# Performance work log

Measured on AMD Instinct MI355X. Metric: run time of the kernel, lower is better.

Reference implementation:

```python
import jax, jax.numpy as jnp
import numpy as np


def _segment_mean(x, idx, num_segments):
    # mean-aggregate rows of x into num_segments buckets (PyG SAGEConv default aggr)
    s = jax.ops.segment_sum(x, idx, num_segments=num_segments)
    c = jax.ops.segment_sum(jnp.ones((idx.shape[0],), x.dtype), idx, num_segments=num_segments)
    return s / jnp.maximum(c, 1.0)[:, None]


def setup_inputs() -> dict:
    key = jax.random.key(0)
    ks = jax.random.split(key, 12)
    N_LIG, N_PROT, D, H, E = 100000, 50000, 64, 128, 2000000
    sc = 0.05
    return {
        "x_lig": jax.random.normal(ks[0], (N_LIG, D), jnp.float32),
        "x_prot": jax.random.normal(ks[1], (N_PROT, D), jnp.float32),
        "W_l_lp": jax.random.normal(ks[2], (D, H), jnp.float32) * sc,
        "b_lp": jnp.zeros((H,), jnp.float32),
        "W_r_lp": jax.random.normal(ks[3], (D, H), jnp.float32) * sc,
        "W_l_pl": jax.random.normal(ks[4], (D, H), jnp.float32) * sc,
        "b_pl": jnp.zeros((H,), jnp.float32),
        "W_r_pl": jax.random.normal(ks[5], (D, H), jnp.float32) * sc,
        "W_lin": jax.random.normal(ks[6], (H, 1), jnp.float32) * sc,
        "b_lin": jnp.zeros((1,), jnp.float32),
        "src_lp": jax.random.randint(ks[7], (E,), 0, N_LIG, jnp.int32),
        "dst_lp": jax.random.randint(ks[8], (E,), 0, N_PROT, jnp.int32),
        "src_pl": jax.random.randint(ks[9], (E,), 0, N_PROT, jnp.int32),
        "dst_pl": jax.random.randint(ks[10], (E,), 0, N_LIG, jnp.int32),
    }


def reference(x_lig, x_prot, W_l_lp, b_lp, W_r_lp, W_l_pl, b_pl, W_r_pl,
              W_lin, b_lin, src_lp, dst_lp, src_pl, dst_pl):
    n_lig = x_lig.shape[0]
    n_prot = x_prot.shape[0]
    # SAGEConv ('ligand','interacts','protein'): gather ligand feats along edges, mean into proteins
    agg_prot = _segment_mean(x_lig[src_lp], dst_lp, n_prot)          # [N_prot, D]
    h_prot = jax.nn.relu(agg_prot @ W_l_lp + b_lp + x_prot @ W_r_lp)  # [N_prot, H] (dead downstream, as in original)
    # SAGEConv ('protein','interacts','ligand')
    agg_lig = _segment_mean(x_prot[src_pl], dst_pl, n_lig)           # [N_lig, D]
    h_lig = jax.nn.relu(agg_lig @ W_l_pl + b_pl + x_lig @ W_r_pl)    # [N_lig, H]
    ligand_out = h_lig.mean(axis=0)                                  # [H]
    del h_prot  # original computes it but never uses it (only 'ligand' feeds the head)
    return ligand_out @ W_lin + b_lin                                # [1]
```

## Files before the change

### kernel.cpp

```cpp
#include <hip/hip_runtime.h>

#define D 64
#define H 128
#define BN 128
#define CAP 3456
#define NBB 512
#define CE 3908

typedef short bf16x8 __attribute__((ext_vector_type(8)));
typedef float f32x4  __attribute__((ext_vector_type(4)));
typedef float f32x2  __attribute__((ext_vector_type(2)));

__device__ __forceinline__ ushort f2bf(float f) {
    unsigned u = __float_as_uint(f);
    unsigned r = (u + 0x7FFFu + ((u >> 16) & 1u)) >> 16;
    return (ushort)r;
}

__device__ __forceinline__ bf16x8 pack8v(f32x4 a, f32x4 b) {
    ushort o[8];
    o[0]=f2bf(a[0]); o[1]=f2bf(a[1]); o[2]=f2bf(a[2]); o[3]=f2bf(a[3]);
    o[4]=f2bf(b[0]); o[5]=f2bf(b[1]); o[6]=f2bf(b[2]); o[7]=f2bf(b[3]);
    bf16x8 r;
    __builtin_memcpy(&r, o, 16);
    return r;
}

__device__ __forceinline__ void acc16(f32x2* a, uint4 v) {
    a[0] += __builtin_amdgcn_cvt_pk_f32_fp8((int)v.x, false);
    a[1] += __builtin_amdgcn_cvt_pk_f32_fp8((int)v.x, true);
    a[2] += __builtin_amdgcn_cvt_pk_f32_fp8((int)v.y, false);
    a[3] += __builtin_amdgcn_cvt_pk_f32_fp8((int)v.y, true);
    a[4] += __builtin_amdgcn_cvt_pk_f32_fp8((int)v.z, false);
    a[5] += __builtin_amdgcn_cvt_pk_f32_fp8((int)v.z, true);
    a[6] += __builtin_amdgcn_cvt_pk_f32_fp8((int)v.w, false);
    a[7] += __builtin_amdgcn_cvt_pk_f32_fp8((int)v.w, true);
}

__device__ __forceinline__ unsigned pk4_fp8(float x0, float x1, float x2, float x3) {
    int w = __builtin_amdgcn_cvt_pk_fp8_f32(x0, x1, 0, false);
    w = __builtin_amdgcn_cvt_pk_fp8_f32(x2, x3, w, true);
    return (unsigned)w;
}

__device__ __forceinline__ int wave_incl_scan(int v, int lane) {
    #pragma unroll
    for (int o = 1; o < 64; o <<= 1) {
        int x = __shfl_up(v, o);
        if (lane >= o) v += x;
    }
    return v;
}

__global__ __launch_bounds__(256)
void stage1_kernel(const float* __restrict__ xp, unsigned char* __restrict__ xp8, int totalp,
                   const float* __restrict__ Wl, const float* __restrict__ Wr,
                   ushort* __restrict__ wprep,
                   const int* __restrict__ dst, int* __restrict__ cnt,
                   int E, int K, int ce, int PB) {
    __shared__ int scnt[800];
    int bid = blockIdx.x;
    int t = threadIdx.x;
    if (bid < PB) {
        int i = (bid * 256 + t) * 16;
        if (i < totalp) {
            const f32x4* p = (const f32x4*)(xp + i);
            f32x4 a = __builtin_nontemporal_load(p);
            f32x4 b = __builtin_nontemporal_load(p + 1);
            f32x4 c = __builtin_nontemporal_load(p + 2);
            f32x4 d = __builtin_nontemporal_load(p + 3);
            uint4 o;
            o.x = pk4_fp8(a[0], a[1], a[2], a[3]);
            o.y = pk4_fp8(b[0], b[1], b[2], b[3]);
            o.z = pk4_fp8(c[0], c[1], c[2], c[3]);
            o.w = pk4_fp8(d[0], d[1], d[2], d[3]);
            *(uint4*)(xp8 + i) = o;
        }
    } else if (bid < PB + 8) {
        int e = (bid - PB) * 256 + t;
        if (e < 2048) {
            int lane = e & 63;
            int ks = (e >> 6) & 3;
            int ht = e >> 8;
            int h = ht * 16 + (lane & 15);
            int kgp = lane >> 4;
            ushort o[8];
            #pragma unroll
            for (int j = 0; j < 8; ++j) {
                int k = (ks < 2) ? (kgp * 16 + ks * 8 + j)
                                 : (ks * 32 + kgp * 8 + j);
                float v = (k < D) ? Wl[k * H + h] : Wr[(k - D) * H + h];
                o[j] = f2bf(v);
            }
            *(bf16x8*)(wprep + (size_t)e * 8) = *(bf16x8*)o;
        }
    } else {
        int blk = bid - PB - 8;
        for (int b = t; b < 800; b += 256) scnt[b] = 0;
        __syncthreads();
        int e0 = blk * ce;
        int e1 = min(E, e0 + ce);
        for (int i = e0 + t * 4; i < e1; i += 1024) {
            int4 d4 = *(const int4*)(dst + i);
            atomicAdd(&scnt[d4.x >> 7], 1);
            atomicAdd(&scnt[d4.y >> 7], 1);
            atomicAdd(&scnt[d4.z >> 7], 1);
            atomicAdd(&scnt[d4.w >> 7], 1);
        }
        __syncthreads();
        int* row = cnt + (size_t)blk * K;
        for (int b = t; b < K; b += 256) row[b] = scnt[b];
    }
}

__global__ __launch_bounds__(NBB)
void part_scan_kernel(const int* __restrict__ cnt, int* __restrict__ off,
                      int* __restrict__ tot, int K) {
    __shared__ int wsum[NBB / 64];
    int b = blockIdx.x;
    int t = threadIdx.x;
    int lane = t & 63, wv = t >> 6;
    int v = cnt[(size_t)t * K + b];
    int incl = wave_incl_scan(v, lane);
    if (lane == 63) wsum[wv] = incl;
    __syncthreads();
    int add = 0;
    #pragma unroll
    for (int w = 0; w < NBB / 64; ++w)
        if (w < wv) add += wsum[w];
    off[(size_t)t * K + b] = incl + add - v;
    if (t == NBB - 1) tot[b] = incl + add;
}

__global__ __launch_bounds__(512)
void part_scatter_kernel(const int* __restrict__ src, const int* __restrict__ dst,
                         const int* __restrict__ off, int* __restrict__ gb,
                         int E, int K, int ce) {
    __shared__ int shist[800];
    __shared__ int sbase[800];
    __shared__ int gdelta[800];
    __shared__ int lcur[800];
    __shared__ int sscan[512];
    __shared__ int ebuf[CE];
    __shared__ unsigned short bkt[CE];

    int blk = blockIdx.x, t = threadIdx.x;
    int e0 = blk * ce;
    int e1 = min(E, e0 + ce);
    int myn = e1 - e0;

    for (int b = t; b < 800; b += 512) shist[b] = 0;
    __syncthreads();
    for (int i = e0 + t * 4; i < e1; i += 2048) {
        int4 d4 = *(const int4*)(dst + i);
        atomicAdd(&shist[d4.x >> 7], 1);
        atomicAdd(&shist[d4.y >> 7], 1);
        atomicAdd(&shist[d4.z >> 7], 1);
        atomicAdd(&shist[d4.w >> 7], 1);
    }
    __syncthreads();
    int c0 = 0, c1 = 0;
    if (t < 400) { c0 = shist[2 * t]; c1 = shist[2 * t + 1]; }
    int cs = c0 + c1;
    sscan[t] = (t < 400) ? cs : 0;
    __syncthreads();
    for (int o = 1; o < 512; o <<= 1) {
        int x = (t >= o) ? sscan[t - o] : 0;
        __syncthreads();
        sscan[t] += x;
        __syncthreads();
    }
    if (t < 400) {
        int ex = sscan[t] - cs;
        sbase[2 * t] = ex;
        sbase[2 * t + 1] = ex + c0;
    }
    __syncthreads();
    const int* orow = off + (size_t)blk * K;
    for (int b = t; b < K; b += 512) {
        int sb = sbase[b];
        gdelta[b] = orow[b] - sb;
        lcur[b] = sb;
    }
    __syncthreads();
    for (int i = e0 + t * 4; i < e1; i += 2048) {
        int4 d4 = *(const int4*)(dst + i);
        int4 s4 = *(const int4*)(src + i);
        int b, p;
        b = d4.x >> 7; p = atomicAdd(&lcur[b], 1);
        ebuf[p] = (s4.x & 0xFFFF) | ((d4.x & 127) << 16); bkt[p] = (unsigned short)b;
        b = d4.y >> 7; p = atomicAdd(&lcur[b], 1);
        ebuf[p] = (s4.y & 0xFFFF) | ((d4.y & 127) << 16); bkt[p] = (unsigned short)b;
        b = d4.z >> 7; p = atomicAdd(&lcur[b], 1);
        ebuf[p] = (s4.z & 0xFFFF) | ((d4.z & 127) << 16); bkt[p] = (unsigned short)b;
        b = d4.w >> 7; p = atomicAdd(&lcur[b], 1);
        ebuf[p] = (s4.w & 0xFFFF) | ((d4.w & 127) << 16); bkt[p] = (unsigned short)b;
    }
    __syncthreads();
    for (int p = t; p < myn; p += 512) {
        int b = bkt[p];
        int loc = gdelta[b] + p;
        if (loc < CAP) gb[(size_t)b * CAP + loc] = ebuf[p];
    }
}

__global__ __launch_bounds__(512, 6)
void fused_kernel(const unsigned char* __restrict__ xp8, const float* __restrict__ x_lig,
                  const int* __restrict__ gtot, const int* __restrict__ gb,
                  const ushort* __restrict__ wprep, const float* __restrict__ bvec,
                  float* __restrict__ pgrid, int N) {
    __shared__ int sdeg[BN];
    __shared__ int sstart[BN];
    __shared__ int scur[BN];
    __shared__ int swtot[2];
    __shared__ int scsr[CAP];
    __shared__ float sred[8][H];

    int b = blockIdx.x, t = threadIdx.x;
    int wv = t >> 6, lane = t & 63;
    int cnt = min(gtot[b], CAP);
    const int* mygb = gb + (size_t)b * CAP;

    if (t < BN) sdeg[t] = 0;
    __syncthreads();
    for (int i = t; i < cnt; i += 512)
        atomicAdd(&sdeg[__builtin_nontemporal_load(&mygb[i]) >> 16], 1);
    __syncthreads();
    int inclv = 0, degv = 0;
    if (t < BN) {
        degv = sdeg[t];
        inclv = wave_incl_scan(degv, lane);
        if (lane == 63) swtot[wv] = inclv;
    }
    __syncthreads();
    if (t < BN) {
        int ex = inclv + ((t >= 64) ? swtot[0] : 0) - degv;
        sstart[t] = ex;
        scur[t] = ex;
    }
    __syncthreads();
    for (int i = t; i < cnt; i += 512) {
        int e = __builtin_nontemporal_load(&mygb[i]);
        int p = atomicAdd(&scur[e >> 16], 1);
        scsr[p] = e & 0xFFFF;
    }
    __syncthreads();

    int r = lane & 15, kg = lane >> 4;

    int ln = wv * 16 + r;
    int s0 = sstart[ln], dg = sdeg[ln];
    f32x2 a[8];
    #pragma unroll
    for (int k = 0; k < 8; ++k) { a[k][0] = 0.f; a[k][1] = 0.f; }
    int j = 0;
    for (; j + 3 < dg; j += 4) {
        int i0 = scsr[s0 + j];
        int i1 = scsr[s0 + j + 1];
        int i2 = scsr[s0 + j + 2];
        int i3 = scsr[s0 + j + 3];
        uint4 v0 = *((const uint4*)(xp8 + (size_t)i0 * D) + kg);
        uint4 v1 = *((const uint4*)(xp8 + (size_t)i1 * D) + kg);
        uint4 v2 = *((const uint4*)(xp8 + (size_t)i2 * D) + kg);
        uint4 v3 = *((const uint4*)(xp8 + (size_t)i3 * D) + kg);
        acc16(a, v0); acc16(a, v1); acc16(a, v2); acc16(a, v3);
    }
    for (; j < dg; ++j) {
        int i0 = scsr[s0 + j];
        uint4 v0 = *((const uint4*)(xp8 + (size_t)i0 * D) + kg);
        acc16(a, v0);
    }

    float inv = 1.0f / fmaxf((float)dg, 1.0f);
    ushort o0[8], o1[8];
    #pragma unroll
    for (int k = 0; k < 4; ++k) {
        o0[2*k]   = f2bf(a[k][0] * inv);
        o0[2*k+1] = f2bf(a[k][1] * inv);
        o1[2*k]   = f2bf(a[4+k][0] * inv);
        o1[2*k+1] = f2bf(a[4+k][1] * inv);
    }
    bf16x8 A0, A1;
    __builtin_memcpy(&A0, o0, 16);
    __builtin_memcpy(&A1, o1, 16);

    int grow = b * BN + wv * 16 + r;
    bf16x8 A2, A3;
    if (grow < N) {
        const f32x4* xr = (const f32x4*)(x_lig + (size_t)grow * D);
        f32x4 va = __builtin_nontemporal_load(xr + kg * 2);
        f32x4 vb = __builtin_nontemporal_load(xr + kg * 2 + 1);
        A2 = pack8v(va, vb);
        f32x4 vc = __builtin_nontemporal_load(xr + 8 + kg * 2);
        f32x4 vd = __builtin_nontemporal_load(xr + 8 + kg * 2 + 1);
        A3 = pack8v(vc, vd);
    } else {
        A2 = bf16x8{0,0,0,0,0,0,0,0};
        A3 = A2;
    }

    float hsum[8];
    bool full = (b * BN + wv * 16 + 16 <= N);
    const bf16x8* wp = (const bf16x8*)wprep;
    #pragma unroll 2
    for (int ht = 0; ht < 8; ++ht) {
        f32x4 acc = {0.f, 0.f, 0.f, 0.f};
        acc = __builtin_amdgcn_mfma_f32_16x16x32_bf16(A0, wp[(ht*4+0)*64 + lane], acc, 0, 0, 0);
        acc = __builtin_amdgcn_mfma_f32_16x16x32_bf16(A1, wp[(ht*4+1)*64 + lane], acc, 0, 0, 0);
        acc = __builtin_amdgcn_mfma_f32_16x16x32_bf16(A2, wp[(ht*4+2)*64 + lane], acc, 0, 0, 0);
        acc = __builtin_amdgcn_mfma_f32_16x16x32_bf16(A3, wp[(ht*4+3)*64 + lane], acc, 0, 0, 0);
        float bb = bvec[ht * 16 + r];
        float s = 0.f;
        if (full) {
            #pragma unroll
            for (int i = 0; i < 4; ++i) s += fmaxf(acc[i] + bb, 0.f);
        } else {
            #pragma unroll
            for (int i = 0; i < 4; ++i) {
                int row = b * BN + wv * 16 + kg * 4 + i;
                if (row < N) s += fmaxf(acc[i] + bb, 0.f);
            }
        }
        hsum[ht] = s;
    }

    #pragma unroll
    for (int ht = 0; ht < 8; ++ht) {
        float v = hsum[ht];
        v += __shfl_xor(v, 16);
        v += __shfl_xor(v, 32);
        if (lane < 16) sred[wv][ht * 16 + lane] = v;
    }
    __syncthreads();
    if (t < H) {
        float s = 0.f;
        #pragma unroll
        for (int w = 0; w < 8; ++w) s += sred[w][t];
        pgrid[(size_t)b * H + t] = s;
    }
}

__global__ __launch_bounds__(128)
void reduce1_kernel(const float* __restrict__ pgrid, int nb, float* __restrict__ pgrid2) {
    int t = threadIdx.x;
    float s = 0.f;
    for (int r = blockIdx.x; r < nb; r += 64) s += pgrid[(size_t)r * H + t];
    pgrid2[(size_t)blockIdx.x * H + t] = s;
}

__global__ __launch_bounds__(128)
void head_kernel(const float* __restrict__ pgrid2,
                 const float* __restrict__ W_lin, const float* __restrict__ b_lin,
                 float* __restrict__ out, float invN) {
    __shared__ float sh[H];
    int t = threadIdx.x;
    float s = 0.f;
    #pragma unroll 8
    for (int r = 0; r < 64; ++r) s += pgrid2[(size_t)r * H + t];
    sh[t] = s * invN * W_lin[t];
    __syncthreads();
    if (t == 0) {
        float tot = b_lin[0];
        for (int i = 0; i < H; ++i) tot += sh[i];
        out[0] = tot;
    }
}

extern "C" void kernel_launch(void* const* d_in, const int* in_sizes, int n_in,
                              void* d_out, int out_size, void* d_ws, size_t ws_size,
                              hipStream_t stream) {
    const float* x_lig  = (const float*)d_in[0];
    const float* x_prot = (const float*)d_in[1];
    const float* W_l_pl = (const float*)d_in[5];
    const float* b_pl   = (const float*)d_in[6];
    const float* W_r_pl = (const float*)d_in[7];
    const float* W_lin  = (const float*)d_in[8];
    const float* b_lin  = (const float*)d_in[9];
    const int*   src_pl = (const int*)d_in[12];
    const int*   dst_pl = (const int*)d_in[13];

    int N  = in_sizes[0] / D;
    int NP = in_sizes[1] / D;
    int E  = in_sizes[12];
    int K  = (N + BN - 1) / BN;

    char* base = (char*)d_ws;
    unsigned char* xp8 = (unsigned char*)base; base += (size_t)NP * D;
    float* pgrid  = (float*)base;   base += (size_t)K * H * sizeof(float);
    float* pgrid2 = (float*)base;   base += (size_t)64 * H * sizeof(float);
    ushort* wprep = (ushort*)base;  base += (size_t)2048 * 8 * sizeof(ushort);
    int* cnt      = (int*)base;     base += (size_t)NBB * K * sizeof(int);
    int* off      = (int*)base;     base += (size_t)NBB * K * sizeof(int);
    int* tot      = (int*)base;     base += (size_t)K * sizeof(int);
    base = (char*)(((size_t)base + 255) & ~(size_t)255);
    int* gb       = (int*)base;     base += (size_t)K * CAP * sizeof(int);

    int ce = ((E + NBB - 1) / NBB + 3) & ~3;
    int PB = (NP * D / 16 + 255) / 256;

    stage1_kernel<<<PB + 8 + NBB, 256, 0, stream>>>(x_prot, xp8, NP * D,
                                                    W_l_pl, W_r_pl, wprep,
                                                    dst_pl, cnt, E, K, ce, PB);
    part_scan_kernel<<<K, NBB, 0, stream>>>(cnt, off, tot, K);
    part_scatter_kernel<<<NBB, 512, 0, stream>>>(src_pl, dst_pl, off, gb, E, K, ce);
    fused_kernel<<<K, 512, 0, stream>>>(xp8, x_lig, tot, gb, wprep, b_pl, pgrid, N);
    reduce1_kernel<<<64, 128, 0, stream>>>(pgrid, K, pgrid2);
    head_kernel<<<1, 128, 0, stream>>>(pgrid2, W_lin, b_lin, (float*)d_out,
                                       1.0f / (float)N);
}
```

Measured before the change: 85.06 us.

## Split each destination bucket across two 256-thread blocks and halve partition blocks

The fused aggregation kernel now launches two 256-thread blocks per 128-row bucket. Each block filters the bucket's edge list to its own 64-row half, builds a smaller shared CSR, and writes its own partial row of the per-block sum grid. NBB also drops from 512 to 256, which gives fewer, larger partition chunks in the scatter stages. The split is meant to raise occupancy and reduce shared memory per block, at the cost of each block reading the full bucket edge list twice. The new CAP2 limit on the shared CSR could drop edges if one half-bucket exceeds 1600 entries.

```diff
diff --git a/kernel.cpp b/kernel.cpp
--- a/kernel.cpp
+++ b/kernel.cpp
@@ -4,8 +4,9 @@
 #define H 128
 #define BN 128
 #define CAP 3456
-#define NBB 512
-#define CE 3908
+#define CAP2 1600
+#define NBB 256
+#define CE 7816
 
 typedef short bf16x8 __attribute__((ext_vector_type(8)));
 typedef float f32x4  __attribute__((ext_vector_type(4)));
@@ -204,48 +205,49 @@
     }
 }
 
-__global__ __launch_bounds__(512, 6)
+__global__ __launch_bounds__(256, 8)
 void fused_kernel(const unsigned char* __restrict__ xp8, const float* __restrict__ x_lig,
                   const int* __restrict__ gtot, const int* __restrict__ gb,
                   const ushort* __restrict__ wprep, const float* __restrict__ bvec,
                   float* __restrict__ pgrid, int N) {
-    __shared__ int sdeg[BN];
-    __shared__ int sstart[BN];
-    __shared__ int scur[BN];
-    __shared__ int swtot[2];
-    __shared__ int scsr[CAP];
-    __shared__ float sred[8][H];
-
-    int b = blockIdx.x, t = threadIdx.x;
-    int wv = t >> 6, lane = t & 63;
-    int cnt = min(gtot[b], CAP);
-    const int* mygb = gb + (size_t)b * CAP;
-
-    if (t < BN) sdeg[t] = 0;
-    __syncthreads();
-    for (int i = t; i < cnt; i += 512)
-        atomicAdd(&sdeg[__builtin_nontemporal_load(&mygb[i]) >> 16], 1);
-    __syncthreads();
-    int inclv = 0, degv = 0;
-    if (t < BN) {
-        degv = sdeg[t];
-        inclv = wave_incl_scan(degv, lane);
-        if (lane == 63) swtot[wv] = inclv;
-    }
-    __syncthreads();
-    if (t < BN) {
-        int ex = inclv + ((t >= 64) ? swtot[0] : 0) - degv;
-        sstart[t] = ex;
-        scur[t] = ex;
-    }
-    __syncthreads();
-    for (int i = t; i < cnt; i += 512) {
+    __shared__ int sdeg[64];
+    __shared__ int sstart[64];
+    __shared__ int scur[64];
+    __shared__ int scsr[CAP2];
+    __shared__ float sred[4][H];
+
+    int blk = blockIdx.x, t = threadIdx.x;
+    int bucket = blk >> 1, half = blk & 1;
+    int cnt = min(gtot[bucket], CAP);
+    const int* mygb = gb + (size_t)bucket * CAP;
+
+    if (t < 64) sdeg[t] = 0;
+    __syncthreads();
+    for (int i = t; i < cnt; i += 256) {
         int e = __builtin_nontemporal_load(&mygb[i]);
-        int p = atomicAdd(&scur[e >> 16], 1);
-        scsr[p] = e & 0xFFFF;
-    }
-    __syncthreads();
-
+        int lb = e >> 16;
+        if ((lb >> 6) == half) atomicAdd(&sdeg[lb & 63], 1);
+    }
+    __syncthreads();
+    int lane = t & 63;
+    if (t < 64) {
+        int degv = sdeg[t];
+        int incl = wave_incl_scan(degv, lane);
+        sstart[t] = incl - degv;
+        scur[t] = incl - degv;
+    }
+    __syncthreads();
+    for (int i = t; i < cnt; i += 256) {
+        int e = __builtin_nontemporal_load(&mygb[i]);
+        int lb = e >> 16;
+        if ((lb >> 6) == half) {
+            int p = atomicAdd(&scur[lb & 63], 1);
+            if (p < CAP2) scsr[p] = e & 0xFFFF;
+        }
+    }
+    __syncthreads();
+
+    int wv = t >> 6;
     int r = lane & 15, kg = lane >> 4;
 
     int ln = wv * 16 + r;
@@ -284,7 +286,7 @@
     __builtin_memcpy(&A0, o0, 16);
     __builtin_memcpy(&A1, o1, 16);
 
-    int grow = b * BN + wv * 16 + r;
+    int grow = blk * 64 + wv * 16 + r;
     bf16x8 A2, A3;
     if (grow < N) {
         const f32x4* xr = (const f32x4*)(x_lig + (size_t)grow * D);
@@ -300,7 +302,7 @@
     }
 
     float hsum[8];
-    bool full = (b * BN + wv * 16 + 16 <= N);
+    bool full = (blk * 64 + wv * 16 + 16 <= N);
     const bf16x8* wp = (const bf16x8*)wprep;
     #pragma unroll 2
     for (int ht = 0; ht < 8; ++ht) {
@@ -317,7 +319,7 @@
         } else {
             #pragma unroll
             for (int i = 0; i < 4; ++i) {
-                int row = b * BN + wv * 16 + kg * 4 + i;
+                int row = blk * 64 + wv * 16 + kg * 4 + i;
                 if (row < N) s += fmaxf(acc[i] + bb, 0.f);
             }
         }
@@ -333,10 +335,8 @@
     }
     __syncthreads();
     if (t < H) {
-        float s = 0.f;
-        #pragma unroll
-        for (int w = 0; w < 8; ++w) s += sred[w][t];
-        pgrid[(size_t)b * H + t] = s;
+        float s = sred[0][t] + sred[1][t] + sred[2][t] + sred[3][t];
+        pgrid[(size_t)blk * H + t] = s;
     }
 }
 
@@ -383,10 +383,11 @@
     int NP = in_sizes[1] / D;
     int E  = in_sizes[12];
     int K  = (N + BN - 1) / BN;
+    int K2 = K * 2;
 
     char* base = (char*)d_ws;
     unsigned char* xp8 = (unsigned char*)base; base += (size_t)NP * D;
-    float* pgrid  = (float*)base;   base += (size_t)K * H * sizeof(float);
+    float* pgrid  = (float*)base;   base += (size_t)K2 * H * sizeof(float);
     float* pgrid2 = (float*)base;   base += (size_t)64 * H * sizeof(float);
     ushort* wprep = (ushort*)base;  base += (size_t)2048 * 8 * sizeof(ushort);
     int* cnt      = (int*)base;     base += (size_t)NBB * K * sizeof(int);
@@ -403,8 +404,8 @@
                                                     dst_pl, cnt, E, K, ce, PB);
     part_scan_kernel<<<K, NBB, 0, stream>>>(cnt, off, tot, K);
     part_scatter_kernel<<<NBB, 512, 0, stream>>>(src_pl, dst_pl, off, gb, E, K, ce);
-    fused_kernel<<<K, 512, 0, stream>>>(xp8, x_lig, tot, gb, wprep, b_pl, pgrid, N);
-    reduce1_kernel<<<64, 128, 0, stream>>>(pgrid, K, pgrid2);
+    fused_kernel<<<K2, 256, 0, stream>>>(xp8, x_lig, tot, gb, wprep, b_pl, pgrid, N);
+    reduce1_kernel<<<64, 128, 0, stream>>>(pgrid, K2, pgrid2);
     head_kernel<<<1, 128, 0, stream>>>(pgrid2, W_lin, b_lin, (float*)d_out,
                                        1.0f / (float)N);
 }
```

New measurement: 110.7 us. 30.1% more time.

## Prefetch edge data into registers and hoist x_lig loads ahead of gather

Applied to the files above, without the earlier changes.

Halves the number of partition blocks (each now handles twice as many edges) and loads all dst indices into registers once, so the histogram and scatter passes reuse them instead of reading global memory twice. In the fused kernel, bucket entries are prefetched into registers before the histogram, so the CSR build reads them once. The x_lig row loads are issued before the neighbor gather loop so their latency overlaps it, and that loop's unroll drops from 4 to 2 to save registers. The trade-offs are higher register pressure, fewer partition blocks, and the fixed register counts (4 int4 per thread, 7 entries) must stay consistent with CE and CAP.

```diff
diff --git a/kernel.cpp b/kernel.cpp
--- a/kernel.cpp
+++ b/kernel.cpp
@@ -4,8 +4,8 @@
 #define H 128
 #define BN 128
 #define CAP 3456
-#define NBB 512
-#define CE 3908
+#define NBB 256
+#define CE 7816
 
 typedef short bf16x8 __attribute__((ext_vector_type(8)));
 typedef float f32x4  __attribute__((ext_vector_type(4)));
@@ -149,14 +149,23 @@
     int e1 = min(E, e0 + ce);
     int myn = e1 - e0;
 
+    int4 dreg[4];
+    #pragma unroll
+    for (int k = 0; k < 4; ++k) {
+        int i = e0 + (t + k * 512) * 4;
+        dreg[k] = (i < e1) ? *(const int4*)(dst + i) : make_int4(-1, -1, -1, -1);
+    }
+
     for (int b = t; b < 800; b += 512) shist[b] = 0;
     __syncthreads();
-    for (int i = e0 + t * 4; i < e1; i += 2048) {
-        int4 d4 = *(const int4*)(dst + i);
-        atomicAdd(&shist[d4.x >> 7], 1);
-        atomicAdd(&shist[d4.y >> 7], 1);
-        atomicAdd(&shist[d4.z >> 7], 1);
-        atomicAdd(&shist[d4.w >> 7], 1);
+    #pragma unroll
+    for (int k = 0; k < 4; ++k) {
+        if (dreg[k].x >= 0) {
+            atomicAdd(&shist[dreg[k].x >> 7], 1);
+            atomicAdd(&shist[dreg[k].y >> 7], 1);
+            atomicAdd(&shist[dreg[k].z >> 7], 1);
+            atomicAdd(&shist[dreg[k].w >> 7], 1);
+        }
     }
     __syncthreads();
     int c0 = 0, c1 = 0;
@@ -183,18 +192,21 @@
         lcur[b] = sb;
     }
     __syncthreads();
-    for (int i = e0 + t * 4; i < e1; i += 2048) {
-        int4 d4 = *(const int4*)(dst + i);
-        int4 s4 = *(const int4*)(src + i);
-        int b, p;
-        b = d4.x >> 7; p = atomicAdd(&lcur[b], 1);
-        ebuf[p] = (s4.x & 0xFFFF) | ((d4.x & 127) << 16); bkt[p] = (unsigned short)b;
-        b = d4.y >> 7; p = atomicAdd(&lcur[b], 1);
-        ebuf[p] = (s4.y & 0xFFFF) | ((d4.y & 127) << 16); bkt[p] = (unsigned short)b;
-        b = d4.z >> 7; p = atomicAdd(&lcur[b], 1);
-        ebuf[p] = (s4.z & 0xFFFF) | ((d4.z & 127) << 16); bkt[p] = (unsigned short)b;
-        b = d4.w >> 7; p = atomicAdd(&lcur[b], 1);
-        ebuf[p] = (s4.w & 0xFFFF) | ((d4.w & 127) << 16); bkt[p] = (unsigned short)b;
+    #pragma unroll
+    for (int k = 0; k < 4; ++k) {
+        int i = e0 + (t + k * 512) * 4;
+        if (dreg[k].x >= 0) {
+            int4 s4 = *(const int4*)(src + i);
+            int b, p;
+            b = dreg[k].x >> 7; p = atomicAdd(&lcur[b], 1);
+            ebuf[p] = (s4.x & 0xFFFF) | ((dreg[k].x & 127) << 16); bkt[p] = (unsigned short)b;
+            b = dreg[k].y >> 7; p = atomicAdd(&lcur[b], 1);
+            ebuf[p] = (s4.y & 0xFFFF) | ((dreg[k].y & 127) << 16); bkt[p] = (unsigned short)b;
+            b = dreg[k].z >> 7; p = atomicAdd(&lcur[b], 1);
+            ebuf[p] = (s4.z & 0xFFFF) | ((dreg[k].z & 127) << 16); bkt[p] = (unsigned short)b;
+            b = dreg[k].w >> 7; p = atomicAdd(&lcur[b], 1);
+            ebuf[p] = (s4.w & 0xFFFF) | ((dreg[k].w & 127) << 16); bkt[p] = (unsigned short)b;
+        }
     }
     __syncthreads();
     for (int p = t; p < myn; p += 512) {
@@ -221,12 +233,20 @@
     int cnt = min(gtot[b], CAP);
     const int* mygb = gb + (size_t)b * CAP;
 
+    int ev[7];
+    #pragma unroll
+    for (int k = 0; k < 7; ++k) {
+        int i = t + k * 512;
+        ev[k] = (i < cnt) ? __builtin_nontemporal_load(&mygb[i]) : -1;
+    }
+
     if (t < BN) sdeg[t] = 0;
     __syncthreads();
-    for (int i = t; i < cnt; i += 512)
-        atomicAdd(&sdeg[__builtin_nontemporal_load(&mygb[i]) >> 16], 1);
-    __syncthreads();
-    int inclv = 0, degv = 0;
+    #pragma unroll
+    for (int k = 0; k < 7; ++k)
+        if (ev[k] >= 0) atomicAdd(&sdeg[ev[k] >> 16], 1);
+    __syncthreads();
+    int degv = 0, inclv = 0;
     if (t < BN) {
         degv = sdeg[t];
         inclv = wave_incl_scan(degv, lane);
@@ -239,14 +259,25 @@
         scur[t] = ex;
     }
     __syncthreads();
-    for (int i = t; i < cnt; i += 512) {
-        int e = __builtin_nontemporal_load(&mygb[i]);
-        int p = atomicAdd(&scur[e >> 16], 1);
-        scsr[p] = e & 0xFFFF;
-    }
+    #pragma unroll
+    for (int k = 0; k < 7; ++k)
+        if (ev[k] >= 0) {
+            int p = atomicAdd(&scur[ev[k] >> 16], 1);
+            scsr[p] = ev[k] & 0xFFFF;
+        }
     __syncthreads();
 
     int r = lane & 15, kg = lane >> 4;
+
+    int grow = b * BN + wv * 16 + r;
+    f32x4 va = {0.f,0.f,0.f,0.f}, vb = va, vc = va, vd = va;
+    if (grow < N) {
+        const f32x4* xr = (const f32x4*)(x_lig + (size_t)grow * D);
+        va = __builtin_nontemporal_load(xr + kg * 2);
+        vb = __builtin_nontemporal_load(xr + kg * 2 + 1);
+        vc = __builtin_nontemporal_load(xr + 8 + kg * 2);
+        vd = __builtin_nontemporal_load(xr + 8 + kg * 2 + 1);
+    }
 
     int ln = wv * 16 + r;
     int s0 = sstart[ln], dg = sdeg[ln];
@@ -254,18 +285,15 @@
     #pragma unroll
     for (int k = 0; k < 8; ++k) { a[k][0] = 0.f; a[k][1] = 0.f; }
     int j = 0;
-    for (; j + 3 < dg; j += 4) {
+    for (; j + 1 < dg; j += 2) {
         int i0 = scsr[s0 + j];
         int i1 = scsr[s0 + j + 1];
-        int i2 = scsr[s0 + j + 2];
-        int i3 = scsr[s0 + j + 3];
         uint4 v0 = *((const uint4*)(xp8 + (size_t)i0 * D) + kg);
         uint4 v1 = *((const uint4*)(xp8 + (size_t)i1 * D) + kg);
-        uint4 v2 = *((const uint4*)(xp8 + (size_t)i2 * D) + kg);
-        uint4 v3 = *((const uint4*)(xp8 + (size_t)i3 * D) + kg);
-        acc16(a, v0); acc16(a, v1); acc16(a, v2); acc16(a, v3);
-    }
-    for (; j < dg; ++j) {
+        acc16(a, v0);
+        acc16(a, v1);
+    }
+    if (j < dg) {
         int i0 = scsr[s0 + j];
         uint4 v0 = *((const uint4*)(xp8 + (size_t)i0 * D) + kg);
         acc16(a, v0);
@@ -284,20 +312,8 @@
     __builtin_memcpy(&A0, o0, 16);
     __builtin_memcpy(&A1, o1, 16);
 
-    int grow = b * BN + wv * 16 + r;
-    bf16x8 A2, A3;
-    if (grow < N) {
-        const f32x4* xr = (const f32x4*)(x_lig + (size_t)grow * D);
-        f32x4 va = __builtin_nontemporal_load(xr + kg * 2);
-        f32x4 vb = __builtin_nontemporal_load(xr + kg * 2 + 1);
-        A2 = pack8v(va, vb);
-        f32x4 vc = __builtin_nontemporal_load(xr + 8 + kg * 2);
-        f32x4 vd = __builtin_nontemporal_load(xr + 8 + kg * 2 + 1);
-        A3 = pack8v(vc, vd);
-    } else {
-        A2 = bf16x8{0,0,0,0,0,0,0,0};
-        A3 = A2;
-    }
+    bf16x8 A2 = pack8v(va, vb);
+    bf16x8 A3 = pack8v(vc, vd);
 
     float hsum[8];
     bool full = (b * BN + wv * 16 + 16 <= N);
```

Result: faster. 79.26 us (-6.8%).
